# Optimization experiments

Hardware: AMD Instinct MI355X
Metric: run time of the kernel (lower is better)

Reference implementation:

```python
import jax, jax.numpy as jnp
import numpy as np

H = 256  # LSTM hidden units per layer

def _cell(xt, h, c, W, U, b):
    # Keras LSTMCell: gate order i, f, g(cell), o; sigmoid recurrent activation, tanh activation
    z = xt @ W + h @ U + b  # (B, 4H)
    i, f, g, o = jnp.split(z, 4, axis=-1)
    c_new = jax.nn.sigmoid(f) * c + jax.nn.sigmoid(i) * jnp.tanh(g)
    h_new = jax.nn.sigmoid(o) * jnp.tanh(c_new)
    return h_new, c_new

def _stacked_lstm(x, W1, U1, b1, W2, U2, b2):
    # x: (B, T, F). Returns concat of FINAL CELL STATES of both layers: (B, 2H)
    # (original code takes outputs[i+1][1], i.e. the c state of each LSTMCell)
    B = x.shape[0]
    def step(carry, xt):
        h1, c1, h2, c2 = carry
        h1, c1 = _cell(xt, h1, c1, W1, U1, b1)
        h2, c2 = _cell(h1, h2, c2, W2, U2, b2)
        return (h1, c1, h2, c2), None
    z0 = jnp.zeros((B, H), x.dtype)
    (h1, c1, h2, c2), _ = jax.lax.scan(step, (z0, z0, z0, z0), jnp.swapaxes(x, 0, 1))
    return jnp.concatenate([c1, c2], axis=-1)

def _glorot(key, shape):
    lim = np.sqrt(6.0 / (shape[0] + shape[1]))
    return jax.random.uniform(key, shape, jnp.float32, -lim, lim)

def _lstm_bias():
    # Keras unit_forget_bias=True: forget-gate bias initialized to 1
    return jnp.zeros((4 * H,), jnp.float32).at[H:2 * H].set(1.0)

def setup_inputs():
    key = jax.random.key(0)
    ks = jax.random.split(key, 16)
    B, T, F, ZD = 16384, 20, 80, 32
    inp = {
        "x": jax.random.normal(ks[0], (B, T, F), jnp.float32),
        "eps1": jax.random.normal(ks[1], (B, ZD), jnp.float32),
        "eps2": jax.random.normal(ks[2], (B, ZD), jnp.float32),
        # z2 stacked LSTM (input F)
        "z2_W1": _glorot(ks[3], (F, 4 * H)), "z2_U1": _glorot(ks[4], (H, 4 * H)), "z2_b1": _lstm_bias(),
        "z2_W2": _glorot(ks[5], (H, 4 * H)), "z2_U2": _glorot(ks[6], (H, 4 * H)), "z2_b2": _lstm_bias(),
        # z1 stacked LSTM (input F + z2_dim)
        "z1_W1": _glorot(ks[7], (F + ZD, 4 * H)), "z1_U1": _glorot(ks[8], (H, 4 * H)), "z1_b1": _lstm_bias(),
        "z1_W2": _glorot(ks[9], (H, 4 * H)), "z1_U2": _glorot(ks[10], (H, 4 * H)), "z1_b2": _lstm_bias(),
        # dense heads (input 2H -> ZD), linear (mu_nl=logvar_nl=None)
        "mu2_W": _glorot(ks[11], (2 * H, ZD)), "mu2_b": jnp.zeros((ZD,), jnp.float32),
        "lv2_W": _glorot(ks[12], (2 * H, ZD)), "lv2_b": jnp.zeros((ZD,), jnp.float32),
        "mu1_W": _glorot(ks[13], (2 * H, ZD)), "mu1_b": jnp.zeros((ZD,), jnp.float32),
        "lv1_W": _glorot(ks[14], (2 * H, ZD)), "lv1_b": jnp.zeros((ZD,), jnp.float32),
    }
    return inp

def reference(x, eps1, eps2,
              z2_W1, z2_U1, z2_b1, z2_W2, z2_U2, z2_b2,
              z1_W1, z1_U1, z1_b1, z1_W2, z1_U2, z1_b2,
              mu2_W, mu2_b, lv2_W, lv2_b, mu1_W, mu1_b, lv1_W, lv1_b):
    B, T, _ = x.shape
    # z2 branch
    z2_pre = _stacked_lstm(x, z2_W1, z2_U1, z2_b1, z2_W2, z2_U2, z2_b2)  # (B, 2H)
    z2_mu = z2_pre @ mu2_W + mu2_b
    z2_logvar = z2_pre @ lv2_W + lv2_b
    z2_sample = eps2 * jnp.exp(0.5 * z2_logvar) + z2_mu  # reparameterize
    # z1 branch: tile z2_sample over time, concat with x
    z2_tiled = jnp.broadcast_to(z2_sample[:, None, :], (B, T, z2_sample.shape[-1]))
    x_z2 = jnp.concatenate([x, z2_tiled], axis=-1)  # (B, T, F+ZD)
    z1_pre = _stacked_lstm(x_z2, z1_W1, z1_U1, z1_b1, z1_W2, z1_U2, z1_b2)
    z1_mu = z1_pre @ mu1_W + mu1_b
    z1_logvar = z1_pre @ lv1_W + lv1_b
    z1_sample = eps1 * jnp.exp(0.5 * z1_logvar) + z1_mu
    return (z1_mu, z1_logvar, z1_sample, z2_mu, z2_logvar, z2_sample)
```

## Files before the change

kernel.cpp:

```cpp
#include <hip/hip_runtime.h>
#include <hip/hip_bf16.h>

#define B_SZ 16384
#define T_SZ 20

typedef __attribute__((ext_vector_type(8))) __bf16 bf16x8;
typedef __attribute__((ext_vector_type(4))) float f32x4;

__device__ __forceinline__ float sigm(float x){ return 1.f/(1.f+__expf(-x)); }
__device__ __forceinline__ float tanh_(float x){ return 1.f-2.f/(__expf(2.f*x)+1.f); }

#define OFF_L1Z2 0
#define OFF_L2Z2 360448
#define OFF_L1Z1 884736
#define OFF_L2Z1 1277952
#define OFF_HZ2  1802240
#define OFF_HZ1  1835008
#define WP_TOT   1867776

__global__ void prep_w(const float* __restrict__ W0, const float* __restrict__ U0,
                       const float* __restrict__ W1, const float* __restrict__ U1,
                       const float* __restrict__ W2, const float* __restrict__ U2,
                       const float* __restrict__ W3, const float* __restrict__ U3,
                       const float* __restrict__ muW2, const float* __restrict__ lvW2,
                       const float* __restrict__ muW1, const float* __restrict__ lvW1,
                       __bf16* __restrict__ wp)
{
    int idx = blockIdx.x * 256 + threadIdx.x;
    if (idx >= WP_TOT) return;
    if (idx < OFF_HZ2) {
        const float *W, *U;
        int Fx, Kx, KT, local;
        if (idx < OFF_L2Z2)      { W = W0; U = U0; Fx = 80;  Kx = 96;  KT = 11; local = idx; }
        else if (idx < OFF_L1Z1) { W = W1; U = U1; Fx = 256; Kx = 256; KT = 16; local = idx - OFF_L2Z2; }
        else if (idx < OFF_L2Z1) { W = W2; U = U2; Fx = 112; Kx = 128; KT = 12; local = idx - OFF_L1Z1; }
        else                     { W = W3; U = U3; Fx = 256; Kx = 256; KT = 16; local = idx - OFF_L2Z1; }
        int jj = local & 7, lane = (local >> 3) & 63, nt16 = (local >> 9) & 15, rest = local >> 13;
        int kt = rest % KT, wgn = rest / KT;
        int gate = nt16 & 3, hh = nt16 >> 2;
        int n = gate * 256 + wgn * 64 + hh * 16 + (lane & 15);
        int k = kt * 32 + ((lane >> 4) << 3) + jj;
        float v = (k < Fx) ? W[k * 1024 + n] : (k < Kx ? 0.f : U[(k - Kx) * 1024 + n]);
        wp[idx] = (__bf16)v;
    } else {
        int base = (idx < OFF_HZ1) ? OFF_HZ2 : OFF_HZ1;
        const float* mw = (idx < OFF_HZ1) ? muW2 : muW1;
        const float* lw = (idx < OFF_HZ1) ? lvW2 : lvW1;
        int local = idx - base;
        int jj = local & 7, lane = (local >> 3) & 63, nt = (local >> 9) & 3, kt = local >> 11;
        int k = kt * 32 + ((lane >> 4) << 3) + jj;
        int c16 = lane & 15;
        float v = (nt < 2) ? mw[k * 32 + nt * 16 + c16] : lw[k * 32 + (nt - 2) * 16 + c16];
        wp[idx] = (__bf16)v;
    }
}

__global__ void xconv(const float* __restrict__ x, __bf16* __restrict__ xb)
{
    int idx = blockIdx.x * 256 + threadIdx.x;
    int c8 = idx & 15, row = idx >> 4;
    bf16x8 r;
    if (c8 < 10) {
        const float4* p = reinterpret_cast<const float4*>(x + (size_t)row * 80 + c8 * 8);
        float4 u0 = p[0], u1 = p[1];
        r[0]=(__bf16)u0.x; r[1]=(__bf16)u0.y; r[2]=(__bf16)u0.z; r[3]=(__bf16)u0.w;
        r[4]=(__bf16)u1.x; r[5]=(__bf16)u1.y; r[6]=(__bf16)u1.z; r[7]=(__bf16)u1.w;
    } else {
#pragma unroll
        for (int i = 0; i < 8; ++i) r[i] = (__bf16)0.f;
    }
    *reinterpret_cast<bf16x8*>(xb + (size_t)row * 128 + c8 * 8) = r;
}

__global__ void bcast_z2(const __bf16* __restrict__ z2sb, __bf16* __restrict__ xb)
{
    int idx = blockIdx.x * 256 + threadIdx.x;
    int g = idx & 3, b = idx >> 2;
    bf16x8 v = *reinterpret_cast<const bf16x8*>(z2sb + (size_t)b * 32 + g * 8);
#pragma unroll
    for (int t = 0; t < T_SZ; ++t)
        *reinterpret_cast<bf16x8*>(xb + ((size_t)b * T_SZ + t) * 128 + 80 + g * 8) = v;
}

__device__ __forceinline__ void stage16(const __bf16* g, __bf16* l)
{
    __builtin_amdgcn_global_load_lds(
        (const __attribute__((address_space(1))) unsigned*)g,
        (__attribute__((address_space(3))) unsigned*)l, 16, 0, 0);
}

template <int KT, int KTP, int XKT, int TWOH, int FIRST>
__device__ __forceinline__ void gemm_step(const __bf16* __restrict__ xb, int t,
          const __bf16* __restrict__ hA, const __bf16* __restrict__ hB,
          const __bf16* __restrict__ wpm, const float* __restrict__ bias,
          float* __restrict__ cbuf, __bf16* __restrict__ hout,
          __bf16 (&As)[3][8192], int bidh)
{
    const int tid = threadIdx.x;
    const int w = tid >> 6, lane = tid & 63;
    const int r16 = lane & 15, kq = lane >> 4;
    const int wr = w >> 2, wc = w & 3;
    const int mid = bidh & 63, wgn = bidh >> 6;
    const int rb = mid * 256;
    const __bf16* wpB = wpm + (size_t)wgn * KTP * 8192;
    const __bf16* pBW = wpB + wc * 2048 + lane * 8;

    const int srow0 = rb + w * 32 + (lane >> 2);
    const int ksub  = (lane & 3) * 8;
    const __bf16* pA0 = hA + (size_t)srow0 * 256 + ksub;
    const __bf16* pA1 = hA + (size_t)(srow0 + 16) * 256 + ksub;
    const __bf16* px0 = (XKT > 0) ? xb + ((size_t)srow0 * T_SZ + t) * 128 + ksub : pA0;
    const __bf16* px1 = (XKT > 0) ? xb + ((size_t)(srow0 + 16) * T_SZ + t) * 128 + ksub : pA1;
    const __bf16* pH0 = TWOH ? hB + (size_t)srow0 * 256 + ksub : pA0;
    const __bf16* pH1 = TWOH ? hB + (size_t)(srow0 + 16) * 256 + ksub : pA1;

    f32x4 acc[4][8];
#pragma unroll
    for (int g = 0; g < 4; ++g)
#pragma unroll
        for (int m = 0; m < 8; ++m) acc[g][m] = f32x4{0.f, 0.f, 0.f, 0.f};

    bf16x8 bR[3][4];

#define ASRC(K, P0, PA, PH_) \
    ((K) < XKT ? (P0) + (K) * 32 \
               : ((!TWOH || ((K) - XKT) < 8) ? (PA) + ((K) - XKT) * 32 \
                                             : (PH_) + ((K) - XKT - 8) * 32))
#define STG_A(K) { stage16(ASRC(K, px0, pA0, pH0), &As[(K) % 3][w * 1024]); \
                   stage16(ASRC(K, px1, pA1, pH1), &As[(K) % 3][w * 1024 + 512]); }
#define LDB(K) { _Pragma("unroll") for (int nt = 0; nt < 4; ++nt) \
                   bR[(K) % 3][nt] = *reinterpret_cast<const bf16x8*>(pBW + (size_t)(K) * 8192 + nt * 512); }
#define CMP(K) { const __bf16* ab_ = &As[(K) % 3][(wr * 128 + r16) * 32 + kq * 8]; \
    bf16x8 a_[8]; \
    _Pragma("unroll") for (int m = 0; m < 8; ++m) \
        a_[m] = *reinterpret_cast<const bf16x8*>(ab_ + m * 512); \
    _Pragma("unroll") for (int m = 0; m < 8; ++m) \
        _Pragma("unroll") for (int g = 0; g < 4; ++g) \
            acc[g][m] = __builtin_amdgcn_mfma_f32_16x16x32_bf16(a_[m], bR[(K) % 3][g], acc[g][m], 0, 0, 0); }
#define PH(K) if constexpr ((K) < KT) { \
    __builtin_amdgcn_sched_barrier(0); \
    if constexpr ((K) + 1 < KT) STG_A((K) + 1); \
    if constexpr ((K) + 2 < KT) LDB((K) + 2); \
    { constexpr int c_ = 2 * (((K) + 1 < KT) ? 1 : 0) + 4 * (((K) + 2 < KT) ? 1 : 0); \
      asm volatile("s_waitcnt vmcnt(%0)" :: "n"(c_) : "memory"); } \
    __builtin_amdgcn_s_barrier(); \
    __builtin_amdgcn_sched_barrier(0); \
    CMP(K); }

    STG_A(0); LDB(0);
    if constexpr (KT > 1) LDB(1);

    PH(0)  PH(1)  PH(2)  PH(3)  PH(4)  PH(5)  PH(6)  PH(7)
    PH(8)  PH(9)  PH(10) PH(11) PH(12) PH(13) PH(14) PH(15)

#undef ASRC
#undef STG_A
#undef LDB
#undef CMP
#undef PH

    const int hcol = wgn * 64 + wc * 16 + r16;
    float bg[4];
#pragma unroll
    for (int g = 0; g < 4; ++g) bg[g] = bias[g * 256 + hcol];

#pragma unroll
    for (int m = 0; m < 8; ++m) {
        f32x4 zi = acc[0][m], zf = acc[1][m], zg = acc[2][m], zo = acc[3][m];
#pragma unroll
        for (int q = 0; q < 4; ++q) {
            int row = rb + wr * 128 + m * 16 + kq * 4 + q;
            size_t off = (size_t)row * 256 + hcol;
            float cn;
            if (FIRST) {
                cn = sigm(zi[q] + bg[0]) * tanh_(zg[q] + bg[2]);
            } else {
                float co = cbuf[off];
                cn = sigm(zf[q] + bg[1]) * co + sigm(zi[q] + bg[0]) * tanh_(zg[q] + bg[2]);
            }
            cbuf[off] = cn;
            hout[off] = (__bf16)(sigm(zo[q] + bg[3]) * tanh_(cn));
        }
    }
}

template <int XKT, int KT1, int PHASE, int FIRST2>
__global__ void __launch_bounds__(512, 2)
fused_step(const __bf16* __restrict__ xb, int t,
           const __bf16* __restrict__ h1cur, __bf16* __restrict__ h1nxt,
           const __bf16* __restrict__ h2prv, __bf16* __restrict__ h2cur,
           const __bf16* __restrict__ wp1, const __bf16* __restrict__ wp2,
           const float* __restrict__ b1, const float* __restrict__ b2,
           float* __restrict__ c1, float* __restrict__ c2)
{
    __shared__ __align__(16) __bf16 As[3][8192];
    const int bidh = blockIdx.x & 255;

    if constexpr (PHASE == 0) {
        gemm_step<XKT, KT1, XKT, 0, 1>(xb, t + 1, h1cur, nullptr, wp1, b1, c1, h1nxt, As, bidh);
    } else if constexpr (PHASE == 2) {
        gemm_step<16, 16, 0, 1, 0>(xb, t, h1cur, h2prv, wp2, b2, c2, h2cur, As, bidh);
    } else {
        if ((blockIdx.x >> 8) == 0) {
            constexpr int KT2 = FIRST2 ? 8 : 16;
            gemm_step<KT2, 16, 0, 1, FIRST2>(xb, t, h1cur, h2prv, wp2, b2, c2, h2cur, As, bidh);
        } else {
            gemm_step<KT1, KT1, XKT, 0, 0>(xb, t + 1, h1cur, nullptr, wp1, b1, c1, h1nxt, As, bidh);
        }
    }
}

__global__ void __launch_bounds__(128, 4)
head_mfma(const float* __restrict__ c1, const float* __restrict__ c2,
          const __bf16* __restrict__ hp, const float* __restrict__ mub,
          const float* __restrict__ lvb, const float* __restrict__ eps,
          float* __restrict__ omu, float* __restrict__ olv, float* __restrict__ osm,
          __bf16* __restrict__ osb)
{
    const int tid = threadIdx.x;
    const int w = tid >> 6, lane = tid & 63;
    const int r16 = lane & 15, kq = lane >> 4;
    const int rb = blockIdx.x * 64 + w * 32;

    f32x4 acc[4][2];
#pragma unroll
    for (int nt = 0; nt < 4; ++nt)
#pragma unroll
        for (int m = 0; m < 2; ++m) acc[nt][m] = f32x4{0.f, 0.f, 0.f, 0.f};

#pragma unroll
    for (int kt = 0; kt < 16; ++kt) {
        const float* cs = (kt < 8) ? c1 : c2;
        int k = (kt & 7) * 32 + kq * 8;
        bf16x8 a[2];
#pragma unroll
        for (int m = 0; m < 2; ++m) {
            const float* pr = cs + (size_t)(rb + m * 16 + r16) * 256 + k;
            float4 u0 = reinterpret_cast<const float4*>(pr)[0];
            float4 u1 = reinterpret_cast<const float4*>(pr)[1];
            a[m][0]=(__bf16)u0.x; a[m][1]=(__bf16)u0.y; a[m][2]=(__bf16)u0.z; a[m][3]=(__bf16)u0.w;
            a[m][4]=(__bf16)u1.x; a[m][5]=(__bf16)u1.y; a[m][6]=(__bf16)u1.z; a[m][7]=(__bf16)u1.w;
        }
        const __bf16* hb = hp + kt * 2048 + lane * 8;
#pragma unroll
        for (int nt = 0; nt < 4; ++nt) {
            bf16x8 bv = *reinterpret_cast<const bf16x8*>(hb + nt * 512);
            acc[nt][0] = __builtin_amdgcn_mfma_f32_16x16x32_bf16(a[0], bv, acc[nt][0], 0, 0, 0);
            acc[nt][1] = __builtin_amdgcn_mfma_f32_16x16x32_bf16(a[1], bv, acc[nt][1], 0, 0, 0);
        }
    }

#pragma unroll
    for (int m = 0; m < 2; ++m)
#pragma unroll
        for (int q = 0; q < 4; ++q) {
            int row = rb + m * 16 + kq * 4 + q;
#pragma unroll
            for (int z = 0; z < 2; ++z) {
                int zc = z * 16 + r16;
                float mu = acc[z][m][q] + mub[zc];
                float lv = acc[z + 2][m][q] + lvb[zc];
                int idx = row * 32 + zc;
                omu[idx] = mu;
                olv[idx] = lv;
                float s = fmaf(eps[idx], expf(0.5f * lv), mu);
                osm[idx] = s;
                if (osb) osb[idx] = (__bf16)s;
            }
        }
}

extern "C" void kernel_launch(void* const* d_in, const int* in_sizes, int n_in,
                              void* d_out, int out_size, void* d_ws, size_t ws_size,
                              hipStream_t stream)
{
    const float* x    = (const float*)d_in[0];
    const float* eps1 = (const float*)d_in[1];
    const float* eps2 = (const float*)d_in[2];
    const float* z2W1 = (const float*)d_in[3];
    const float* z2U1 = (const float*)d_in[4];
    const float* z2b1 = (const float*)d_in[5];
    const float* z2W2 = (const float*)d_in[6];
    const float* z2U2 = (const float*)d_in[7];
    const float* z2b2 = (const float*)d_in[8];
    const float* z1W1 = (const float*)d_in[9];
    const float* z1U1 = (const float*)d_in[10];
    const float* z1b1 = (const float*)d_in[11];
    const float* z1W2 = (const float*)d_in[12];
    const float* z1U2 = (const float*)d_in[13];
    const float* z1b2 = (const float*)d_in[14];
    const float* mu2W = (const float*)d_in[15];
    const float* mu2b = (const float*)d_in[16];
    const float* lv2W = (const float*)d_in[17];
    const float* lv2b = (const float*)d_in[18];
    const float* mu1W = (const float*)d_in[19];
    const float* mu1b = (const float*)d_in[20];
    const float* lv1W = (const float*)d_in[21];
    const float* lv1b = (const float*)d_in[22];

    char* ws = (char*)d_ws;
    __bf16* wp   = (__bf16*)ws;
    __bf16* z2sb = (__bf16*)(ws + 4194304);
    __bf16* xb   = (__bf16*)(ws + 5242880);
    __bf16* h1a  = (__bf16*)(ws + 89128960);
    __bf16* h1b  = (__bf16*)(ws + 97517568);
    __bf16* h2a  = (__bf16*)(ws + 105906176);
    __bf16* h2b  = (__bf16*)(ws + 114294784);
    float*  c1   = (float*)(ws + 122683392);
    float*  c2   = (float*)(ws + 139460608);

    __bf16* h1[2] = {h1a, h1b};
    __bf16* h2[2] = {h2a, h2b};

    float* out = (float*)d_out;
    const int BZ = B_SZ * 32;
    float* z1mu = out;           float* z1lv = out + BZ;     float* z1sm = out + 2 * BZ;
    float* z2mu = out + 3 * BZ;  float* z2lv = out + 4 * BZ; float* z2sm = out + 5 * BZ;

    xconv<<<B_SZ * T_SZ * 16 / 256, 256, 0, stream>>>(x, xb);
    prep_w<<<7296, 256, 0, stream>>>(z2W1, z2U1, z2W2, z2U2, z1W1, z1U1, z1W2, z1U2,
                                     mu2W, lv2W, mu1W, lv1W, wp);

    {
        const __bf16* wpa = wp + OFF_L1Z2;
        const __bf16* wpb = wp + OFF_L2Z2;
        fused_step<3, 11, 0, 0><<<256, 512, 0, stream>>>(xb, -1, h1[0], h1[0], h2[0], h2[0],
                                                         wpa, wpb, z2b1, z2b2, c1, c2);
        fused_step<3, 11, 1, 1><<<512, 512, 0, stream>>>(xb, 0, h1[0], h1[1], h2[1], h2[0],
                                                         wpa, wpb, z2b1, z2b2, c1, c2);
        for (int t = 1; t < T_SZ - 1; ++t)
            fused_step<3, 11, 1, 0><<<512, 512, 0, stream>>>(xb, t, h1[t & 1], h1[(t + 1) & 1],
                                                             h2[(t + 1) & 1], h2[t & 1],
                                                             wpa, wpb, z2b1, z2b2, c1, c2);
        fused_step<3, 11, 2, 0><<<256, 512, 0, stream>>>(xb, 19, h1[1], h1[0], h2[0], h2[1],
                                                         wpa, wpb, z2b1, z2b2, c1, c2);
    }
    head_mfma<<<256, 128, 0, stream>>>(c1, c2, wp + OFF_HZ2, mu2b, lv2b, eps2,
                                       z2mu, z2lv, z2sm, z2sb);
    bcast_z2<<<B_SZ * 4 / 256, 256, 0, stream>>>(z2sb, xb);

    {
        const __bf16* wpa = wp + OFF_L1Z1;
        const __bf16* wpb = wp + OFF_L2Z1;
        fused_step<4, 12, 0, 0><<<256, 512, 0, stream>>>(xb, -1, h1[0], h1[0], h2[0], h2[0],
                                                         wpa, wpb, z1b1, z1b2, c1, c2);
        fused_step<4, 12, 1, 1><<<512, 512, 0, stream>>>(xb, 0, h1[0], h1[1], h2[1], h2[0],
                                                         wpa, wpb, z1b1, z1b2, c1, c2);
        for (int t = 1; t < T_SZ - 1; ++t)
            fused_step<4, 12, 1, 0><<<512, 512, 0, stream>>>(xb, t, h1[t & 1], h1[(t + 1) & 1],
                                                             h2[(t + 1) & 1], h2[t & 1],
                                                             wpa, wpb, z1b1, z1b2, c1, c2);
        fused_step<4, 12, 2, 0><<<256, 512, 0, stream>>>(xb, 19, h1[1], h1[0], h2[0], h2[1],
                                                         wpa, wpb, z1b1, z1b2, c1, c2);
    }
    head_mfma<<<256, 128, 0, stream>>>(c1, c2, wp + OFF_HZ1, mu1b, lv1b, eps1,
                                       z1mu, z1lv, z1sm, nullptr);
}
```

Measured before the change: 2.069 ms.

## Deepen A-tile LDS pipeline to four buffers, swizzle LDS layout, raise MFMA priority

Moves the A-tile global-to-LDS staging two k-steps ahead, matching the B register prefetch, and grows the LDS ring buffer from three to four slots. The vmcnt waits are recomputed to fit the deeper in-flight window. It also XOR-swizzles the 16-byte k-chunk position on both the staging and the read side to cut LDS bank conflicts on the MFMA operand reads. CMP is wrapped in s_setprio so MFMA work is favoured over other waves. The cost is more LDS per block (64KB), which may limit occupancy at 2 blocks per CU.

```diff
diff --git a/kernel.cpp b/kernel.cpp
--- a/kernel.cpp
+++ b/kernel.cpp
@@ -94,7 +94,7 @@
           const __bf16* __restrict__ hA, const __bf16* __restrict__ hB,
           const __bf16* __restrict__ wpm, const float* __restrict__ bias,
           float* __restrict__ cbuf, __bf16* __restrict__ hout,
-          __bf16 (&As)[3][8192], int bidh)
+          __bf16 (&As)[4][8192], int bidh)
 {
     const int tid = threadIdx.x;
     const int w = tid >> 6, lane = tid & 63;
@@ -106,13 +106,13 @@
     const __bf16* pBW = wpB + wc * 2048 + lane * 8;
 
     const int srow0 = rb + w * 32 + (lane >> 2);
-    const int ksub  = (lane & 3) * 8;
-    const __bf16* pA0 = hA + (size_t)srow0 * 256 + ksub;
-    const __bf16* pA1 = hA + (size_t)(srow0 + 16) * 256 + ksub;
-    const __bf16* px0 = (XKT > 0) ? xb + ((size_t)srow0 * T_SZ + t) * 128 + ksub : pA0;
-    const __bf16* px1 = (XKT > 0) ? xb + ((size_t)(srow0 + 16) * T_SZ + t) * 128 + ksub : pA1;
-    const __bf16* pH0 = TWOH ? hB + (size_t)srow0 * 256 + ksub : pA0;
-    const __bf16* pH1 = TWOH ? hB + (size_t)(srow0 + 16) * 256 + ksub : pA1;
+    const int ksw   = (((lane & 3) ^ ((lane >> 3) & 3)) << 3);
+    const __bf16* pA0 = hA + (size_t)srow0 * 256 + ksw;
+    const __bf16* pA1 = hA + (size_t)(srow0 + 16) * 256 + ksw;
+    const __bf16* px0 = (XKT > 0) ? xb + ((size_t)srow0 * T_SZ + t) * 128 + ksw : pA0;
+    const __bf16* px1 = (XKT > 0) ? xb + ((size_t)(srow0 + 16) * T_SZ + t) * 128 + ksw : pA1;
+    const __bf16* pH0 = TWOH ? hB + (size_t)srow0 * 256 + ksw : pA0;
+    const __bf16* pH1 = TWOH ? hB + (size_t)(srow0 + 16) * 256 + ksw : pA1;
 
     f32x4 acc[4][8];
 #pragma unroll
@@ -121,16 +121,17 @@
         for (int m = 0; m < 8; ++m) acc[g][m] = f32x4{0.f, 0.f, 0.f, 0.f};
 
     bf16x8 bR[3][4];
+    const int slotA = ((kq ^ ((r16 >> 1) & 3)) << 3);
 
 #define ASRC(K, P0, PA, PH_) \
     ((K) < XKT ? (P0) + (K) * 32 \
                : ((!TWOH || ((K) - XKT) < 8) ? (PA) + ((K) - XKT) * 32 \
                                              : (PH_) + ((K) - XKT - 8) * 32))
-#define STG_A(K) { stage16(ASRC(K, px0, pA0, pH0), &As[(K) % 3][w * 1024]); \
-                   stage16(ASRC(K, px1, pA1, pH1), &As[(K) % 3][w * 1024 + 512]); }
+#define STG_A(K) { stage16(ASRC(K, px0, pA0, pH0), &As[(K) & 3][w * 1024]); \
+                   stage16(ASRC(K, px1, pA1, pH1), &As[(K) & 3][w * 1024 + 512]); }
 #define LDB(K) { _Pragma("unroll") for (int nt = 0; nt < 4; ++nt) \
                    bR[(K) % 3][nt] = *reinterpret_cast<const bf16x8*>(pBW + (size_t)(K) * 8192 + nt * 512); }
-#define CMP(K) { const __bf16* ab_ = &As[(K) % 3][(wr * 128 + r16) * 32 + kq * 8]; \
+#define CMP(K) { const __bf16* ab_ = &As[(K) & 3][(wr * 128 + r16) * 32 + slotA]; \
     bf16x8 a_[8]; \
     _Pragma("unroll") for (int m = 0; m < 8; ++m) \
         a_[m] = *reinterpret_cast<const bf16x8*>(ab_ + m * 512); \
@@ -139,16 +140,17 @@
             acc[g][m] = __builtin_amdgcn_mfma_f32_16x16x32_bf16(a_[m], bR[(K) % 3][g], acc[g][m], 0, 0, 0); }
 #define PH(K) if constexpr ((K) < KT) { \
     __builtin_amdgcn_sched_barrier(0); \
-    if constexpr ((K) + 1 < KT) STG_A((K) + 1); \
-    if constexpr ((K) + 2 < KT) LDB((K) + 2); \
-    { constexpr int c_ = 2 * (((K) + 1 < KT) ? 1 : 0) + 4 * (((K) + 2 < KT) ? 1 : 0); \
+    if constexpr ((K) + 2 < KT) { STG_A((K) + 2); LDB((K) + 2); } \
+    { constexpr int c_ = 6 * (((K) + 1 < KT) ? 1 : 0) + 6 * (((K) + 2 < KT) ? 1 : 0); \
       asm volatile("s_waitcnt vmcnt(%0)" :: "n"(c_) : "memory"); } \
     __builtin_amdgcn_s_barrier(); \
     __builtin_amdgcn_sched_barrier(0); \
-    CMP(K); }
+    __builtin_amdgcn_s_setprio(1); \
+    CMP(K); \
+    __builtin_amdgcn_s_setprio(0); }
 
     STG_A(0); LDB(0);
-    if constexpr (KT > 1) LDB(1);
+    if constexpr (KT > 1) { STG_A(1); LDB(1); }
 
     PH(0)  PH(1)  PH(2)  PH(3)  PH(4)  PH(5)  PH(6)  PH(7)
     PH(8)  PH(9)  PH(10) PH(11) PH(12) PH(13) PH(14) PH(15)
@@ -193,7 +195,7 @@
            const float* __restrict__ b1, const float* __restrict__ b2,
            float* __restrict__ c1, float* __restrict__ c2)
 {
-    __shared__ __align__(16) __bf16 As[3][8192];
+    __shared__ __align__(16) __bf16 As[4][8192];
     const int bidh = blockIdx.x & 255;
 
     if constexpr (PHASE == 0) {
```

Measured after the change: 2.074 ms. About the same (+0.3%).

## Remap warp tiling to 4x2 and cut B prefetch depth to one stage

Applied to the files above, without the earlier changes.

Changes the per-wave output tile from 128 rows x 16 hidden columns (4 gates) to 64 rows x 32 hidden columns. Each wave now reads half as many A fragments from LDS per K-step but loads twice as many B (weight) fragments from global memory. The B register prefetch buffer shrinks from a 3-deep to a 2-deep ring, and loads go from two steps ahead to one. This trades less LDS traffic for more global/L2 weight traffic, and the shallower prefetch may expose more load latency.

```diff
diff --git a/kernel.cpp b/kernel.cpp
--- a/kernel.cpp
+++ b/kernel.cpp
@@ -99,11 +99,11 @@
     const int tid = threadIdx.x;
     const int w = tid >> 6, lane = tid & 63;
     const int r16 = lane & 15, kq = lane >> 4;
-    const int wr = w >> 2, wc = w & 3;
+    const int wr = w >> 1, wc = w & 1;
     const int mid = bidh & 63, wgn = bidh >> 6;
     const int rb = mid * 256;
     const __bf16* wpB = wpm + (size_t)wgn * KTP * 8192;
-    const __bf16* pBW = wpB + wc * 2048 + lane * 8;
+    const __bf16* pBW = wpB + wc * 4096 + lane * 8;
 
     const int srow0 = rb + w * 32 + (lane >> 2);
     const int ksub  = (lane & 3) * 8;
@@ -114,13 +114,13 @@
     const __bf16* pH0 = TWOH ? hB + (size_t)srow0 * 256 + ksub : pA0;
     const __bf16* pH1 = TWOH ? hB + (size_t)(srow0 + 16) * 256 + ksub : pA1;
 
-    f32x4 acc[4][8];
-#pragma unroll
-    for (int g = 0; g < 4; ++g)
-#pragma unroll
-        for (int m = 0; m < 8; ++m) acc[g][m] = f32x4{0.f, 0.f, 0.f, 0.f};
-
-    bf16x8 bR[3][4];
+    f32x4 acc[8][4];
+#pragma unroll
+    for (int j = 0; j < 8; ++j)
+#pragma unroll
+        for (int m = 0; m < 4; ++m) acc[j][m] = f32x4{0.f, 0.f, 0.f, 0.f};
+
+    bf16x8 bR[2][8];
 
 #define ASRC(K, P0, PA, PH_) \
     ((K) < XKT ? (P0) + (K) * 32 \
@@ -128,27 +128,25 @@
                                              : (PH_) + ((K) - XKT - 8) * 32))
 #define STG_A(K) { stage16(ASRC(K, px0, pA0, pH0), &As[(K) % 3][w * 1024]); \
                    stage16(ASRC(K, px1, pA1, pH1), &As[(K) % 3][w * 1024 + 512]); }
-#define LDB(K) { _Pragma("unroll") for (int nt = 0; nt < 4; ++nt) \
-                   bR[(K) % 3][nt] = *reinterpret_cast<const bf16x8*>(pBW + (size_t)(K) * 8192 + nt * 512); }
-#define CMP(K) { const __bf16* ab_ = &As[(K) % 3][(wr * 128 + r16) * 32 + kq * 8]; \
-    bf16x8 a_[8]; \
-    _Pragma("unroll") for (int m = 0; m < 8; ++m) \
+#define LDB(K) { _Pragma("unroll") for (int nt = 0; nt < 8; ++nt) \
+                   bR[(K) & 1][nt] = *reinterpret_cast<const bf16x8*>(pBW + (size_t)(K) * 8192 + nt * 512); }
+#define CMP(K) { const __bf16* ab_ = &As[(K) % 3][(wr * 64 + r16) * 32 + kq * 8]; \
+    bf16x8 a_[4]; \
+    _Pragma("unroll") for (int m = 0; m < 4; ++m) \
         a_[m] = *reinterpret_cast<const bf16x8*>(ab_ + m * 512); \
-    _Pragma("unroll") for (int m = 0; m < 8; ++m) \
-        _Pragma("unroll") for (int g = 0; g < 4; ++g) \
-            acc[g][m] = __builtin_amdgcn_mfma_f32_16x16x32_bf16(a_[m], bR[(K) % 3][g], acc[g][m], 0, 0, 0); }
+    _Pragma("unroll") for (int m = 0; m < 4; ++m) \
+        _Pragma("unroll") for (int j = 0; j < 8; ++j) \
+            acc[j][m] = __builtin_amdgcn_mfma_f32_16x16x32_bf16(a_[m], bR[(K) & 1][j], acc[j][m], 0, 0, 0); }
 #define PH(K) if constexpr ((K) < KT) { \
     __builtin_amdgcn_sched_barrier(0); \
-    if constexpr ((K) + 1 < KT) STG_A((K) + 1); \
-    if constexpr ((K) + 2 < KT) LDB((K) + 2); \
-    { constexpr int c_ = 2 * (((K) + 1 < KT) ? 1 : 0) + 4 * (((K) + 2 < KT) ? 1 : 0); \
+    if constexpr ((K) + 1 < KT) { STG_A((K) + 1); LDB((K) + 1); } \
+    { constexpr int c_ = ((K) + 1 < KT) ? 10 : 0; \
       asm volatile("s_waitcnt vmcnt(%0)" :: "n"(c_) : "memory"); } \
     __builtin_amdgcn_s_barrier(); \
     __builtin_amdgcn_sched_barrier(0); \
     CMP(K); }
 
     STG_A(0); LDB(0);
-    if constexpr (KT > 1) LDB(1);
 
     PH(0)  PH(1)  PH(2)  PH(3)  PH(4)  PH(5)  PH(6)  PH(7)
     PH(8)  PH(9)  PH(10) PH(11) PH(12) PH(13) PH(14) PH(15)
@@ -159,29 +157,35 @@
 #undef CMP
 #undef PH
 
-    const int hcol = wgn * 64 + wc * 16 + r16;
-    float bg[4];
-#pragma unroll
-    for (int g = 0; g < 4; ++g) bg[g] = bias[g * 256 + hcol];
-
-#pragma unroll
-    for (int m = 0; m < 8; ++m) {
-        f32x4 zi = acc[0][m], zf = acc[1][m], zg = acc[2][m], zo = acc[3][m];
-#pragma unroll
-        for (int q = 0; q < 4; ++q) {
-            int row = rb + wr * 128 + m * 16 + kq * 4 + q;
-            size_t off = (size_t)row * 256 + hcol;
-            float cn;
-            if (FIRST) {
-                cn = sigm(zi[q] + bg[0]) * tanh_(zg[q] + bg[2]);
-            } else {
-                float co = cbuf[off];
-                cn = sigm(zf[q] + bg[1]) * co + sigm(zi[q] + bg[0]) * tanh_(zg[q] + bg[2]);
+    const int hcb = wgn * 64 + wc * 32;
+    float bg[2][4];
+#pragma unroll
+    for (int hh = 0; hh < 2; ++hh)
+#pragma unroll
+        for (int g = 0; g < 4; ++g) bg[hh][g] = bias[g * 256 + hcb + hh * 16 + r16];
+
+#pragma unroll
+    for (int m = 0; m < 4; ++m)
+#pragma unroll
+        for (int hh = 0; hh < 2; ++hh) {
+            const int hcol = hcb + hh * 16 + r16;
+            f32x4 zi = acc[hh * 4 + 0][m], zf = acc[hh * 4 + 1][m];
+            f32x4 zg = acc[hh * 4 + 2][m], zo = acc[hh * 4 + 3][m];
+#pragma unroll
+            for (int q = 0; q < 4; ++q) {
+                int row = rb + wr * 64 + m * 16 + kq * 4 + q;
+                size_t off = (size_t)row * 256 + hcol;
+                float cn;
+                if (FIRST) {
+                    cn = sigm(zi[q] + bg[hh][0]) * tanh_(zg[q] + bg[hh][2]);
+                } else {
+                    float co = cbuf[off];
+                    cn = sigm(zf[q] + bg[hh][1]) * co + sigm(zi[q] + bg[hh][0]) * tanh_(zg[q] + bg[hh][2]);
+                }
+                cbuf[off] = cn;
+                hout[off] = (__bf16)(sigm(zo[q] + bg[hh][3]) * tanh_(cn));
             }
-            cbuf[off] = cn;
-            hout[off] = (__bf16)(sigm(zo[q] + bg[3]) * tanh_(cn));
-        }
-    }
+        }
 }
 
 template <int XKT, int KT1, int PHASE, int FIRST2>
```

Result: no change. 2.096 ms (+1.3%).
